# Performance work log

Hardware: AMD Instinct MI355X
Metric: run time of the kernel (lower is better)

The kernel has to match this reference:

```python
import jax, jax.numpy as jnp
import numpy as np

H = 16        # n_heads
D = 1024      # d_model
SPLIT = 4     # number of sequence blocks, each with its own MHA weights
DK = D // H   # head dim
B = 4
SEQ = 4096


def setup_inputs() -> dict:
    key = jax.random.key(0)
    ks = jax.random.split(key, 9)
    sc = 1.0 / np.sqrt(D).astype(np.float32)
    x = jax.random.normal(ks[0], (B, SEQ, D), jnp.float32)
    # Per-split projection weights (torch Linear applied as x @ W + b; random init so
    # the transpose convention is immaterial for a correctness baseline).
    Wq = jax.random.normal(ks[1], (SPLIT, D, D), jnp.float32) * sc
    Wk = jax.random.normal(ks[2], (SPLIT, D, D), jnp.float32) * sc
    Wv = jax.random.normal(ks[3], (SPLIT, D, D), jnp.float32) * sc
    Wo = jax.random.normal(ks[4], (SPLIT, D, D), jnp.float32) * sc
    bq = jax.random.normal(ks[5], (SPLIT, D), jnp.float32) * 0.02
    bk = jax.random.normal(ks[6], (SPLIT, D), jnp.float32) * 0.02
    bv = jax.random.normal(ks[7], (SPLIT, D), jnp.float32) * 0.02
    bo = jax.random.normal(ks[8], (SPLIT, D), jnp.float32) * 0.02
    return {"x": x, "Wq": Wq, "Wk": Wk, "Wv": Wv, "Wo": Wo,
            "bq": bq, "bk": bk, "bv": bv, "bo": bo}


def reference(x, Wq, Wk, Wv, Wo, bq, bk, bv, bo):
    b, l, d = x.shape
    L = l // SPLIT                     # block length
    xs = x.reshape(b, SPLIT, L, d)     # [b, s, L, d] block-diagonal structure

    def proj(W, bias):
        return jnp.einsum('bsld,sde->bsle', xs, W) + bias[None, :, None, :]

    q = proj(Wq, bq).reshape(b, SPLIT, L, H, DK)
    k = proj(Wk, bk).reshape(b, SPLIT, L, H, DK)
    v = proj(Wv, bv).reshape(b, SPLIT, L, H, DK)

    # scaled dot-product attention within each block, causal mask per block
    scores = jnp.einsum('bslhk,bsmhk->bshlm', q, k) / np.sqrt(DK).astype(np.float32)
    causal = jnp.tril(jnp.ones((L, L), dtype=bool))
    scores = jnp.where(causal[None, None, None], scores, jnp.float32(-1e9))
    attn = jax.nn.softmax(scores, axis=-1)   # dropout is identity in eval mode
    o = jnp.einsum('bshlm,bsmhk->bslhk', attn, v).reshape(b, SPLIT, L, d)

    out = jnp.einsum('bsld,sde->bsle', o, Wo) + bo[None, :, None, :]
    return out.reshape(b, l, d)
```

## Files before the change

kernel.cpp:

```cpp
#include <hip/hip_runtime.h>
#include <stdint.h>

#define H_ 16
#define D_ 1024
#define SPLIT_ 4
#define DK_ 64
#define B_ 4
#define SEQ_ 4096
#define L_ 1024

#define QSC 0.18033688f

typedef unsigned short ushort_t;
typedef __attribute__((ext_vector_type(8))) short short8;
typedef __attribute__((ext_vector_type(4))) float floatx4;
typedef __attribute__((ext_vector_type(4))) unsigned short ushortx4;

__device__ __forceinline__ ushort_t f2bf(float f) {
  union { float f; unsigned u; } cv; cv.f = f;
  unsigned u = cv.u;
  return (ushort_t)((u + 0x7fffu + ((u >> 16) & 1u)) >> 16);
}

__device__ __forceinline__ uint32_t pack_bf_trunc(float x, float y) {
#if __has_builtin(__builtin_amdgcn_perm)
  return __builtin_amdgcn_perm(__float_as_uint(y), __float_as_uint(x), 0x07060302u);
#else
  return (__float_as_uint(y) & 0xffff0000u) | (__float_as_uint(x) >> 16);
#endif
}

__device__ __forceinline__ float exp2f_fast(float x) {
#if __has_builtin(__builtin_amdgcn_exp2f)
  return __builtin_amdgcn_exp2f(x);
#else
  return exp2f(x);
#endif
}

__device__ __forceinline__ void gl2lds16(const ushort_t* g, ushort_t* l) {
  __builtin_amdgcn_global_load_lds(
      (const __attribute__((address_space(1))) uint32_t*)g,
      (__attribute__((address_space(3))) uint32_t*)l, 16, 0, 0);
}

__global__ __launch_bounds__(256) void convert_x(const float* __restrict__ X,
                                                 ushort_t* __restrict__ Y) {
  const int i = blockIdx.x * 256 + threadIdx.x;
  const float4 v = ((const float4*)X)[i];
  ushortx4 o;
  o[0] = f2bf(v.x); o[1] = f2bf(v.y); o[2] = f2bf(v.z); o[3] = f2bf(v.w);
  ((ushortx4*)Y)[i] = o;
}

__global__ __launch_bounds__(256) void wt_convert_all(const float* __restrict__ W0,
                                                      const float* __restrict__ W1,
                                                      const float* __restrict__ W2,
                                                      const float* __restrict__ W3,
                                                      ushort_t* __restrict__ Wt) {
  __shared__ ushort_t tile[32][33];
  const int z = blockIdx.z, mat = z >> 2, s = z & 3;
  const float* W = (mat == 0) ? W0 : (mat == 1) ? W1 : (mat == 2) ? W2 : W3;
  const float scale = (mat == 0) ? QSC : 1.0f;
  const float* Ws = W + (size_t)s * D_ * D_;
  ushort_t* Wts = Wt + ((size_t)mat * SPLIT_ + s) * D_ * D_;
  const int e0 = blockIdx.x * 32, d0 = blockIdx.y * 32;
  for (int i = threadIdx.y; i < 32; i += 8)
    tile[i][threadIdx.x] = f2bf(Ws[(size_t)(d0 + i) * D_ + e0 + threadIdx.x] * scale);
  __syncthreads();
  for (int i = threadIdx.y; i < 32; i += 8)
    Wts[(size_t)(e0 + i) * D_ + d0 + threadIdx.x] = tile[threadIdx.x][i];
}

template <int MODE>
__global__ __launch_bounds__(256) void gemm_bt(const ushort_t* __restrict__ X,
                                               const ushort_t* __restrict__ Wt,
                                               const float* __restrict__ bias,
                                               float bscale,
                                               void* __restrict__ Cv) {
  __shared__ __attribute__((aligned(16))) ushort_t SH[8192];
  ushort_t* As = SH;
  ushort_t* Bs = SH + 4096;

  const int bs = blockIdx.z;
  const int s = bs & 3;
  const int m0 = blockIdx.y * 128;
  const int n0 = blockIdx.x * 128;
  const ushort_t* Xb = X + (size_t)bs * (L_ * D_);
  const ushort_t* Wts = Wt + (size_t)s * (D_ * D_);

  const int t = threadIdx.x;
  const int lane = t & 63;
  const int w = t >> 6;
  const int wm = w >> 1, wn = w & 1;
  const int quad = lane >> 4, cl = lane & 15;

  floatx4 acc[4][4];
  floatx4 zero = {0.f, 0.f, 0.f, 0.f};
#pragma unroll
  for (int i = 0; i < 4; ++i)
#pragma unroll
    for (int j = 0; j < 4; ++j) acc[i][j] = zero;

  const int c0 = t, c1 = t + 256;
  const int r0 = c0 >> 2, cc0 = ((c0 & 3) ^ (r0 & 3)) * 8;
  const int r1 = c1 >> 2, cc1 = ((c1 & 3) ^ (r1 & 3)) * 8;
  const int sw = (quad ^ (cl & 3)) * 8;

  for (int k0 = 0; k0 < D_; k0 += 32) {
    gl2lds16(Xb + (size_t)(m0 + r0) * D_ + k0 + cc0, &As[c0 * 8]);
    gl2lds16(Xb + (size_t)(m0 + r1) * D_ + k0 + cc1, &As[c1 * 8]);
    gl2lds16(Wts + (size_t)(n0 + r0) * D_ + k0 + cc0, &Bs[c0 * 8]);
    gl2lds16(Wts + (size_t)(n0 + r1) * D_ + k0 + cc1, &Bs[c1 * 8]);
    __syncthreads();
    short8 a[4], b[4];
#pragma unroll
    for (int i = 0; i < 4; ++i)
      a[i] = *(const short8*)&As[(wm * 64 + i * 16 + cl) * 32 + sw];
#pragma unroll
    for (int j = 0; j < 4; ++j)
      b[j] = *(const short8*)&Bs[(wn * 64 + j * 16 + cl) * 32 + sw];
#pragma unroll
    for (int i = 0; i < 4; ++i)
#pragma unroll
      for (int j = 0; j < 4; ++j)
        acc[i][j] = __builtin_amdgcn_mfma_f32_16x16x32_bf16(a[i], b[j], acc[i][j], 0, 0, 0);
    __syncthreads();
  }

  float bvj[4];
#pragma unroll
  for (int j = 0; j < 4; ++j)
    bvj[j] = bias[s * D_ + n0 + wn * 64 + j * 16 + cl] * bscale;

  if (MODE == 2) {
#pragma unroll
    for (int j = 0; j < 4; ++j) {
      const int col = n0 + wn * 64 + j * 16 + cl;
#pragma unroll
      for (int i = 0; i < 4; ++i) {
        const int rb = m0 + wm * 64 + i * 16 + quad * 4;
        float* Cf = (float*)Cv + (size_t)bs * (L_ * D_) + (size_t)rb * D_ + col;
#pragma unroll
        for (int r = 0; r < 4; ++r) Cf[(size_t)r * D_] = acc[i][j][r] + bvj[j];
      }
    }
    return;
  }

  ushort_t* CT = SH;
#pragma unroll
  for (int ph = 0; ph < 2; ++ph) {
    __syncthreads();
    if (MODE == 0 ? (wm == ph) : (wn == ph)) {
#pragma unroll
      for (int i = 0; i < 4; ++i)
#pragma unroll
        for (int j = 0; j < 4; ++j)
#pragma unroll
          for (int r = 0; r < 4; ++r) {
            int row, col;
            if (MODE == 0) { row = i * 16 + quad * 4 + r; col = wn * 64 + j * 16 + cl; }
            else           { row = j * 16 + cl;           col = wm * 64 + i * 16 + quad * 4 + r; }
            const int ch = col >> 3, off = col & 7;
            CT[row * 128 + ((ch ^ (row & 15)) << 3) + off] = f2bf(acc[i][j][r] + bvj[j]);
          }
    }
    __syncthreads();
#pragma unroll
    for (int pass = 0; pass < 4; ++pass) {
      const int row = pass * 16 + (t >> 4);
      const int ck = t & 15;
      const short8 v = *(const short8*)&CT[row * 128 + ((ck ^ (row & 15)) << 3)];
      if (MODE == 0) {
        *(short8*)((ushort_t*)Cv + (size_t)bs * (L_ * D_) +
                   (size_t)(m0 + ph * 64 + row) * D_ + n0 + ck * 8) = v;
      } else {
        *(short8*)((ushort_t*)Cv + (size_t)bs * (L_ * D_) +
                   (size_t)(n0 + ph * 64 + row) * L_ + m0 + ck * 8) = v;
      }
    }
  }
}

__global__ __launch_bounds__(256) void attn_kernel(const ushort_t* __restrict__ Q,
                                                   const ushort_t* __restrict__ K,
                                                   const ushort_t* __restrict__ Vt,
                                                   ushort_t* __restrict__ O) {
  __shared__ __attribute__((aligned(16))) ushort_t Ks[2][64 * 64];
  __shared__ __attribute__((aligned(16))) ushort_t Vts[2][64 * 64];
  __shared__ __attribute__((aligned(16))) ushort_t PT[4][1152];

  const int p = blockIdx.x, h = blockIdx.y, bs = blockIdx.z;
  const int t = threadIdx.x, lane = t & 63, w = t >> 6;
  const int quad = lane >> 4, cl = lane & 15;
  const size_t act_base = (size_t)bs * (L_ * D_);
  const int qtA = p, qtB = 15 - p;
  const int seg1 = p + 1;
  const int NIT = 17;

  const int cA = t, cB = t + 256;
  const int rA = cA >> 3, ccA = ((cA & 7) ^ (rA & 7)) * 8;
  const int rB = cB >> 3, ccB = ((cB & 7) ^ (rB & 7)) * 8;

  const ushort_t* kbaseA = K + act_base + (size_t)rA * D_ + h * DK_ + ccA;
  const ushort_t* kbaseB = K + act_base + (size_t)rB * D_ + h * DK_ + ccB;
  const ushort_t* vbaseA = Vt + act_base + (size_t)(h * DK_ + rA) * L_ + ccA;
  const ushort_t* vbaseB = Vt + act_base + (size_t)(h * DK_ + rB) * L_ + ccB;
  const ushort_t *pKA = kbaseA, *pKB = kbaseB, *pVA = vbaseA, *pVB = vbaseB;
  const size_t kstep = (size_t)64 * D_, vstep = 64;

  floatx4 zero = {0.f, 0.f, 0.f, 0.f};
  short8 qa0, qa1;
  floatx4 o[4];
  float m_i, l_i;
  int qt = qtA;

  gl2lds16(pKA, &Ks[0][cA * 8]);
  gl2lds16(pKB, &Ks[0][cB * 8]);
  gl2lds16(pVA, &Vts[0][cA * 8]);
  gl2lds16(pVB, &Vts[0][cB * 8]);

  for (int i = 0; i < NIT; ++i) {
    __syncthreads();
    if (i + 1 < NIT) {
      const int nk = (i + 1 < seg1) ? i + 1 : i + 1 - seg1;
      if (nk == 0) { pKA = kbaseA; pKB = kbaseB; pVA = vbaseA; pVB = vbaseB; }
      else { pKA += kstep; pKB += kstep; pVA += vstep; pVB += vstep; }
      const int nb = (i + 1) & 1;
      gl2lds16(pKA, &Ks[nb][cA * 8]);
      gl2lds16(pKB, &Ks[nb][cB * 8]);
      gl2lds16(pVA, &Vts[nb][cA * 8]);
      gl2lds16(pVB, &Vts[nb][cB * 8]);
    }
    const int buf = i & 1;

    if (i == 0 || i == seg1) {
      qt = (i == 0) ? qtA : qtB;
      const ushort_t* Qp = Q + act_base + (size_t)(qt * 64 + w * 16 + cl) * D_ + h * DK_ + quad * 8;
      qa0 = *(const short8*)Qp;
      qa1 = *(const short8*)(Qp + 32);
#pragma unroll
      for (int j = 0; j < 4; ++j) o[j] = zero;
      m_i = -3.0e38f; l_i = 0.f;
    }
    const bool segend = (i == seg1 - 1) || (i == NIT - 1);

    floatx4 st[4];
#pragma unroll
    for (int j = 0; j < 4; ++j) {
      const int row = (j * 16 + cl) * 64;
      const short8 ka0 = *(const short8*)&Ks[buf][row + ((quad ^ (cl & 7)) * 8)];
      const short8 ka1 = *(const short8*)&Ks[buf][row + (((4 + quad) ^ (cl & 7)) * 8)];
      floatx4 z = zero;
      z = __builtin_amdgcn_mfma_f32_16x16x32_bf16(ka0, qa0, z, 0, 0, 0);
      z = __builtin_amdgcn_mfma_f32_16x16x32_bf16(ka1, qa1, z, 0, 0, 0);
      st[j] = z;
    }

    if (segend) {
      const int ql = w * 16 + cl;
#pragma unroll
      for (int j = 0; j < 4; ++j)
#pragma unroll
        for (int r = 0; r < 4; ++r)
          if (j * 16 + quad * 4 + r > ql) st[j][r] = -1e30f;
    }

    float tm = fmaxf(fmaxf(fmaxf(st[0][0], st[0][1]), fmaxf(st[0][2], st[0][3])),
                     fmaxf(fmaxf(st[1][0], st[1][1]), fmaxf(st[1][2], st[1][3])));
    tm = fmaxf(tm, fmaxf(fmaxf(fmaxf(st[2][0], st[2][1]), fmaxf(st[2][2], st[2][3])),
                         fmaxf(fmaxf(st[3][0], st[3][1]), fmaxf(st[3][2], st[3][3]))));
    tm = fmaxf(tm, __shfl_xor(tm, 16, 64));
    tm = fmaxf(tm, __shfl_xor(tm, 32, 64));
    const float mnew = fmaxf(m_i, tm);
    const float alpha = exp2f_fast(m_i - mnew);
    m_i = mnew;

    float tsv = 0.f;
#pragma unroll
    for (int j = 0; j < 4; ++j)
#pragma unroll
      for (int r = 0; r < 4; ++r) {
        st[j][r] = exp2f_fast(st[j][r] - mnew);
        tsv += st[j][r];
      }
    tsv += __shfl_xor(tsv, 16, 64);
    tsv += __shfl_xor(tsv, 32, 64);
    l_i = l_i * alpha + tsv;

#pragma unroll
    for (int j = 0; j < 4; ++j) {
      const int base = cl * 72 + j * 16 + quad * 4;
      *(uint32_t*)&PT[w][base] = pack_bf_trunc(st[j][0], st[j][1]);
      *(uint32_t*)&PT[w][base + 2] = pack_bf_trunc(st[j][2], st[j][3]);
    }

#pragma unroll
    for (int j = 0; j < 4; ++j)
#pragma unroll
      for (int r = 0; r < 4; ++r) o[j][r] *= alpha;

    const short8 pb0 = *(const short8*)&PT[w][cl * 72 + quad * 8];
    const short8 pb1 = *(const short8*)&PT[w][cl * 72 + 32 + quad * 8];
#pragma unroll
    for (int j = 0; j < 4; ++j) {
      const int row = (j * 16 + cl) * 64;
      const short8 va0 = *(const short8*)&Vts[buf][row + ((quad ^ (cl & 7)) * 8)];
      const short8 va1 = *(const short8*)&Vts[buf][row + (((4 + quad) ^ (cl & 7)) * 8)];
      o[j] = __builtin_amdgcn_mfma_f32_16x16x32_bf16(va0, pb0, o[j], 0, 0, 0);
      o[j] = __builtin_amdgcn_mfma_f32_16x16x32_bf16(va1, pb1, o[j], 0, 0, 0);
    }

    if (segend) {
      const float inv = 1.0f / l_i;
      ushort_t* Orow = O + act_base + (size_t)(qt * 64 + w * 16 + cl) * D_ + h * DK_;
#pragma unroll
      for (int j = 0; j < 4; ++j) {
        ushortx4 pk;
#pragma unroll
        for (int r = 0; r < 4; ++r) pk[r] = f2bf(o[j][r] * inv);
        *(ushortx4*)(Orow + j * 16 + quad * 4) = pk;
      }
    }
  }
}

extern "C" void kernel_launch(void* const* d_in, const int* in_sizes, int n_in,
                              void* d_out, int out_size, void* d_ws, size_t ws_size,
                              hipStream_t stream) {
  const float* x  = (const float*)d_in[0];
  const float* Wq = (const float*)d_in[1];
  const float* Wk = (const float*)d_in[2];
  const float* Wv = (const float*)d_in[3];
  const float* Wo = (const float*)d_in[4];
  const float* bq = (const float*)d_in[5];
  const float* bk = (const float*)d_in[6];
  const float* bv = (const float*)d_in[7];
  const float* bo = (const float*)d_in[8];

  const size_t WT_SZ = (size_t)SPLIT_ * D_ * D_;
  const size_t ACT_SZ = (size_t)B_ * SEQ_ * D_;

  ushort_t* ws0 = (ushort_t*)d_ws;
  ushort_t* xbf = ws0;
  ushort_t* wtall = xbf + ACT_SZ;
  ushort_t* wtq = wtall;
  ushort_t* wtk = wtq + WT_SZ;
  ushort_t* wtv = wtk + WT_SZ;
  ushort_t* wto = wtv + WT_SZ;
  ushort_t* Vtb = wto + WT_SZ;
  ushort_t* Qb = (ushort_t*)d_out;
  ushort_t* Kb = Qb + ACT_SZ;
  ushort_t* Ob = xbf;

  convert_x<<<ACT_SZ / 1024, 256, 0, stream>>>(x, xbf);
  wt_convert_all<<<dim3(32, 32, 16), dim3(32, 8, 1), 0, stream>>>(Wq, Wk, Wv, Wo, wtall);

  dim3 gb(256, 1, 1), gg(8, 8, 16);
  gemm_bt<0><<<gg, gb, 0, stream>>>(xbf, wtq, bq, QSC, Qb);
  gemm_bt<0><<<gg, gb, 0, stream>>>(xbf, wtk, bk, 1.0f, Kb);
  gemm_bt<1><<<gg, gb, 0, stream>>>(xbf, wtv, bv, 1.0f, Vtb);

  dim3 ag(8, 16, 16);
  attn_kernel<<<ag, dim3(256, 1, 1), 0, stream>>>(Qb, Kb, Vtb, Ob);

  gemm_bt<2><<<gg, gb, 0, stream>>>(Ob, wto, bo, 1.0f, d_out);
}
```

Measured before the change: 507.2 us.

## Share K/V tile loads across paired query tiles and remap GEMM grid for XCD locality

The attention kernel now processes both paired query tiles (p and 15-p) in the same pass over K/V tiles. Each loaded K/V tile is used by both query tiles, so K/V traffic for the shared prefix is no longer loaded twice and the iteration count drops from 17 to 16-p. It keeps two sets of accumulators, which raises register pressure and doubles the PT scratch in LDS. Separately, the GEMM grid is re-indexed so consecutive block IDs, which are likely spread across XCDs, map to different batch-splits, with each XCD covering one batch-split's tiles for L2 locality.

```diff
diff --git a/kernel.cpp b/kernel.cpp
--- a/kernel.cpp
+++ b/kernel.cpp
@@ -82,10 +82,13 @@
   ushort_t* As = SH;
   ushort_t* Bs = SH + 4096;
 
-  const int bs = blockIdx.z;
+  const int xcd = blockIdx.x;
+  const int u = blockIdx.y;
+  const int bs = xcd + ((u >> 6) << 3);
+  const int mn = u & 63;
+  const int m0 = (mn >> 3) * 128;
+  const int n0 = (mn & 7) * 128;
   const int s = bs & 3;
-  const int m0 = blockIdx.y * 128;
-  const int n0 = blockIdx.x * 128;
   const ushort_t* Xb = X + (size_t)bs * (L_ * D_);
   const ushort_t* Wts = Wt + (size_t)s * (D_ * D_);
 
@@ -183,147 +186,163 @@
   }
 }
 
+__device__ __forceinline__ void attn_step(const ushort_t* __restrict__ Kbuf,
+                                          const ushort_t* __restrict__ Vbuf,
+                                          ushort_t* __restrict__ PTw,
+                                          const short8 qa0, const short8 qa1,
+                                          floatx4 (&o)[4], float& m_i, float& l_i,
+                                          const bool diag, const int w,
+                                          const int quad, const int cl) {
+  floatx4 zero = {0.f, 0.f, 0.f, 0.f};
+  const int sw0 = (quad ^ (cl & 7)) * 8;
+  const int sw1 = ((4 + quad) ^ (cl & 7)) * 8;
+
+  floatx4 st[4];
+#pragma unroll
+  for (int j = 0; j < 4; ++j) {
+    const int row = (j * 16 + cl) * 64;
+    const short8 ka0 = *(const short8*)&Kbuf[row + sw0];
+    const short8 ka1 = *(const short8*)&Kbuf[row + sw1];
+    floatx4 z = zero;
+    z = __builtin_amdgcn_mfma_f32_16x16x32_bf16(ka0, qa0, z, 0, 0, 0);
+    z = __builtin_amdgcn_mfma_f32_16x16x32_bf16(ka1, qa1, z, 0, 0, 0);
+    st[j] = z;
+  }
+
+  if (diag) {
+    const int ql = w * 16 + cl;
+#pragma unroll
+    for (int j = 0; j < 4; ++j)
+#pragma unroll
+      for (int r = 0; r < 4; ++r)
+        if (j * 16 + quad * 4 + r > ql) st[j][r] = -1e30f;
+  }
+
+  float tm = fmaxf(fmaxf(fmaxf(st[0][0], st[0][1]), fmaxf(st[0][2], st[0][3])),
+                   fmaxf(fmaxf(st[1][0], st[1][1]), fmaxf(st[1][2], st[1][3])));
+  tm = fmaxf(tm, fmaxf(fmaxf(fmaxf(st[2][0], st[2][1]), fmaxf(st[2][2], st[2][3])),
+                       fmaxf(fmaxf(st[3][0], st[3][1]), fmaxf(st[3][2], st[3][3]))));
+  tm = fmaxf(tm, __shfl_xor(tm, 16, 64));
+  tm = fmaxf(tm, __shfl_xor(tm, 32, 64));
+  const float mnew = fmaxf(m_i, tm);
+  const float alpha = exp2f_fast(m_i - mnew);
+  m_i = mnew;
+
+  float tsv = 0.f;
+#pragma unroll
+  for (int j = 0; j < 4; ++j)
+#pragma unroll
+    for (int r = 0; r < 4; ++r) {
+      st[j][r] = exp2f_fast(st[j][r] - mnew);
+      tsv += st[j][r];
+    }
+  tsv += __shfl_xor(tsv, 16, 64);
+  tsv += __shfl_xor(tsv, 32, 64);
+  l_i = l_i * alpha + tsv;
+
+#pragma unroll
+  for (int j = 0; j < 4; ++j) {
+    const int base = cl * 72 + j * 16 + quad * 4;
+    *(uint32_t*)&PTw[base] = pack_bf_trunc(st[j][0], st[j][1]);
+    *(uint32_t*)&PTw[base + 2] = pack_bf_trunc(st[j][2], st[j][3]);
+  }
+
+#pragma unroll
+  for (int j = 0; j < 4; ++j)
+#pragma unroll
+    for (int r = 0; r < 4; ++r) o[j][r] *= alpha;
+
+  const short8 pb0 = *(const short8*)&PTw[cl * 72 + quad * 8];
+  const short8 pb1 = *(const short8*)&PTw[cl * 72 + 32 + quad * 8];
+#pragma unroll
+  for (int j = 0; j < 4; ++j) {
+    const int row = (j * 16 + cl) * 64;
+    const short8 va0 = *(const short8*)&Vbuf[row + sw0];
+    const short8 va1 = *(const short8*)&Vbuf[row + sw1];
+    o[j] = __builtin_amdgcn_mfma_f32_16x16x32_bf16(va0, pb0, o[j], 0, 0, 0);
+    o[j] = __builtin_amdgcn_mfma_f32_16x16x32_bf16(va1, pb1, o[j], 0, 0, 0);
+  }
+}
+
+__device__ __forceinline__ void attn_store(ushort_t* __restrict__ O, size_t act_base,
+                                           int qt, int h, const floatx4 (&o)[4],
+                                           float l_i, int w, int quad, int cl) {
+  const float inv = 1.0f / l_i;
+  ushort_t* Orow = O + act_base + (size_t)(qt * 64 + w * 16 + cl) * D_ + h * DK_;
+#pragma unroll
+  for (int j = 0; j < 4; ++j) {
+    ushortx4 pk;
+#pragma unroll
+    for (int r = 0; r < 4; ++r) pk[r] = f2bf(o[j][r] * inv);
+    *(ushortx4*)(Orow + j * 16 + quad * 4) = pk;
+  }
+}
+
 __global__ __launch_bounds__(256) void attn_kernel(const ushort_t* __restrict__ Q,
                                                    const ushort_t* __restrict__ K,
                                                    const ushort_t* __restrict__ Vt,
                                                    ushort_t* __restrict__ O) {
   __shared__ __attribute__((aligned(16))) ushort_t Ks[2][64 * 64];
   __shared__ __attribute__((aligned(16))) ushort_t Vts[2][64 * 64];
-  __shared__ __attribute__((aligned(16))) ushort_t PT[4][1152];
+  __shared__ __attribute__((aligned(16))) ushort_t PT[8][1152];
 
   const int p = blockIdx.x, h = blockIdx.y, bs = blockIdx.z;
   const int t = threadIdx.x, lane = t & 63, w = t >> 6;
   const int quad = lane >> 4, cl = lane & 15;
   const size_t act_base = (size_t)bs * (L_ * D_);
   const int qtA = p, qtB = 15 - p;
-  const int seg1 = p + 1;
-  const int NIT = 17;
+  const int NIT = 16 - p;
 
   const int cA = t, cB = t + 256;
   const int rA = cA >> 3, ccA = ((cA & 7) ^ (rA & 7)) * 8;
   const int rB = cB >> 3, ccB = ((cB & 7) ^ (rB & 7)) * 8;
 
-  const ushort_t* kbaseA = K + act_base + (size_t)rA * D_ + h * DK_ + ccA;
-  const ushort_t* kbaseB = K + act_base + (size_t)rB * D_ + h * DK_ + ccB;
-  const ushort_t* vbaseA = Vt + act_base + (size_t)(h * DK_ + rA) * L_ + ccA;
-  const ushort_t* vbaseB = Vt + act_base + (size_t)(h * DK_ + rB) * L_ + ccB;
-  const ushort_t *pKA = kbaseA, *pKB = kbaseB, *pVA = vbaseA, *pVB = vbaseB;
+  const ushort_t* pKA = K + act_base + (size_t)rA * D_ + h * DK_ + ccA;
+  const ushort_t* pKB = K + act_base + (size_t)rB * D_ + h * DK_ + ccB;
+  const ushort_t* pVA = Vt + act_base + (size_t)(h * DK_ + rA) * L_ + ccA;
+  const ushort_t* pVB = Vt + act_base + (size_t)(h * DK_ + rB) * L_ + ccB;
   const size_t kstep = (size_t)64 * D_, vstep = 64;
 
   floatx4 zero = {0.f, 0.f, 0.f, 0.f};
-  short8 qa0, qa1;
-  floatx4 o[4];
-  float m_i, l_i;
-  int qt = qtA;
+
+  const ushort_t* QpA = Q + act_base + (size_t)(qtA * 64 + w * 16 + cl) * D_ + h * DK_ + quad * 8;
+  const ushort_t* QpB = Q + act_base + (size_t)(qtB * 64 + w * 16 + cl) * D_ + h * DK_ + quad * 8;
+  const short8 qaA0 = *(const short8*)QpA;
+  const short8 qaA1 = *(const short8*)(QpA + 32);
+  const short8 qaB0 = *(const short8*)QpB;
+  const short8 qaB1 = *(const short8*)(QpB + 32);
+
+  floatx4 oA[4], oB[4];
+#pragma unroll
+  for (int j = 0; j < 4; ++j) { oA[j] = zero; oB[j] = zero; }
+  float mA = -3.0e38f, lA = 0.f, mB = -3.0e38f, lB = 0.f;
 
   gl2lds16(pKA, &Ks[0][cA * 8]);
   gl2lds16(pKB, &Ks[0][cB * 8]);
   gl2lds16(pVA, &Vts[0][cA * 8]);
   gl2lds16(pVB, &Vts[0][cB * 8]);
 
-  for (int i = 0; i < NIT; ++i) {
-    __syncthreads();
-    if (i + 1 < NIT) {
-      const int nk = (i + 1 < seg1) ? i + 1 : i + 1 - seg1;
-      if (nk == 0) { pKA = kbaseA; pKB = kbaseB; pVA = vbaseA; pVB = vbaseB; }
-      else { pKA += kstep; pKB += kstep; pVA += vstep; pVB += vstep; }
-      const int nb = (i + 1) & 1;
+  for (int kv = 0; kv < NIT; ++kv) {
+    __syncthreads();
+    if (kv + 1 < NIT) {
+      pKA += kstep; pKB += kstep; pVA += vstep; pVB += vstep;
+      const int nb = (kv + 1) & 1;
       gl2lds16(pKA, &Ks[nb][cA * 8]);
       gl2lds16(pKB, &Ks[nb][cB * 8]);
       gl2lds16(pVA, &Vts[nb][cA * 8]);
       gl2lds16(pVB, &Vts[nb][cB * 8]);
     }
-    const int buf = i & 1;
-
-    if (i == 0 || i == seg1) {
-      qt = (i == 0) ? qtA : qtB;
-      const ushort_t* Qp = Q + act_base + (size_t)(qt * 64 + w * 16 + cl) * D_ + h * DK_ + quad * 8;
-      qa0 = *(const short8*)Qp;
-      qa1 = *(const short8*)(Qp + 32);
-#pragma unroll
-      for (int j = 0; j < 4; ++j) o[j] = zero;
-      m_i = -3.0e38f; l_i = 0.f;
-    }
-    const bool segend = (i == seg1 - 1) || (i == NIT - 1);
-
-    floatx4 st[4];
-#pragma unroll
-    for (int j = 0; j < 4; ++j) {
-      const int row = (j * 16 + cl) * 64;
-      const short8 ka0 = *(const short8*)&Ks[buf][row + ((quad ^ (cl & 7)) * 8)];
-      const short8 ka1 = *(const short8*)&Ks[buf][row + (((4 + quad) ^ (cl & 7)) * 8)];
-      floatx4 z = zero;
-      z = __builtin_amdgcn_mfma_f32_16x16x32_bf16(ka0, qa0, z, 0, 0, 0);
-      z = __builtin_amdgcn_mfma_f32_16x16x32_bf16(ka1, qa1, z, 0, 0, 0);
-      st[j] = z;
-    }
-
-    if (segend) {
-      const int ql = w * 16 + cl;
-#pragma unroll
-      for (int j = 0; j < 4; ++j)
-#pragma unroll
-        for (int r = 0; r < 4; ++r)
-          if (j * 16 + quad * 4 + r > ql) st[j][r] = -1e30f;
-    }
-
-    float tm = fmaxf(fmaxf(fmaxf(st[0][0], st[0][1]), fmaxf(st[0][2], st[0][3])),
-                     fmaxf(fmaxf(st[1][0], st[1][1]), fmaxf(st[1][2], st[1][3])));
-    tm = fmaxf(tm, fmaxf(fmaxf(fmaxf(st[2][0], st[2][1]), fmaxf(st[2][2], st[2][3])),
-                         fmaxf(fmaxf(st[3][0], st[3][1]), fmaxf(st[3][2], st[3][3]))));
-    tm = fmaxf(tm, __shfl_xor(tm, 16, 64));
-    tm = fmaxf(tm, __shfl_xor(tm, 32, 64));
-    const float mnew = fmaxf(m_i, tm);
-    const float alpha = exp2f_fast(m_i - mnew);
-    m_i = mnew;
-
-    float tsv = 0.f;
-#pragma unroll
-    for (int j = 0; j < 4; ++j)
-#pragma unroll
-      for (int r = 0; r < 4; ++r) {
-        st[j][r] = exp2f_fast(st[j][r] - mnew);
-        tsv += st[j][r];
-      }
-    tsv += __shfl_xor(tsv, 16, 64);
-    tsv += __shfl_xor(tsv, 32, 64);
-    l_i = l_i * alpha + tsv;
-
-#pragma unroll
-    for (int j = 0; j < 4; ++j) {
-      const int base = cl * 72 + j * 16 + quad * 4;
-      *(uint32_t*)&PT[w][base] = pack_bf_trunc(st[j][0], st[j][1]);
-      *(uint32_t*)&PT[w][base + 2] = pack_bf_trunc(st[j][2], st[j][3]);
-    }
-
-#pragma unroll
-    for (int j = 0; j < 4; ++j)
-#pragma unroll
-      for (int r = 0; r < 4; ++r) o[j][r] *= alpha;
-
-    const short8 pb0 = *(const short8*)&PT[w][cl * 72 + quad * 8];
-    const short8 pb1 = *(const short8*)&PT[w][cl * 72 + 32 + quad * 8];
-#pragma unroll
-    for (int j = 0; j < 4; ++j) {
-      const int row = (j * 16 + cl) * 64;
-      const short8 va0 = *(const short8*)&Vts[buf][row + ((quad ^ (cl & 7)) * 8)];
-      const short8 va1 = *(const short8*)&Vts[buf][row + (((4 + quad) ^ (cl & 7)) * 8)];
-      o[j] = __builtin_amdgcn_mfma_f32_16x16x32_bf16(va0, pb0, o[j], 0, 0, 0);
-      o[j] = __builtin_amdgcn_mfma_f32_16x16x32_bf16(va1, pb1, o[j], 0, 0, 0);
-    }
-
-    if (segend) {
-      const float inv = 1.0f / l_i;
-      ushort_t* Orow = O + act_base + (size_t)(qt * 64 + w * 16 + cl) * D_ + h * DK_;
-#pragma unroll
-      for (int j = 0; j < 4; ++j) {
-        ushortx4 pk;
-#pragma unroll
-        for (int r = 0; r < 4; ++r) pk[r] = f2bf(o[j][r] * inv);
-        *(ushortx4*)(Orow + j * 16 + quad * 4) = pk;
-      }
-    }
-  }
+    const int buf = kv & 1;
+
+    if (kv <= p) {
+      attn_step(Ks[buf], Vts[buf], PT[w], qaA0, qaA1, oA, mA, lA,
+                kv == p, w, quad, cl);
+      if (kv == p) attn_store(O, act_base, qtA, h, oA, lA, w, quad, cl);
+    }
+    attn_step(Ks[buf], Vts[buf], PT[w + 4], qaB0, qaB1, oB, mB, lB,
+              kv == NIT - 1, w, quad, cl);
+  }
+  attn_store(O, act_base, qtB, h, oB, lB, w, quad, cl);
 }
 
 extern "C" void kernel_launch(void* const* d_in, const int* in_sizes, int n_in,
@@ -357,7 +376,7 @@
   convert_x<<<ACT_SZ / 1024, 256, 0, stream>>>(x, xbf);
   wt_convert_all<<<dim3(32, 32, 16), dim3(32, 8, 1), 0, stream>>>(Wq, Wk, Wv, Wo, wtall);
 
-  dim3 gb(256, 1, 1), gg(8, 8, 16);
+  dim3 gb(256, 1, 1), gg(8, 128, 1);
   gemm_bt<0><<<gg, gb, 0, stream>>>(xbf, wtq, bq, QSC, Qb);
   gemm_bt<0><<<gg, gb, 0, stream>>>(xbf, wtk, bk, 1.0f, Kb);
   gemm_bt<1><<<gg, gb, 0, stream>>>(xbf, wtv, bv, 1.0f, Vtb);
```

Result: faster. 470.2 us (-7.3%).
